# Kernel tuning notes

Measured on AMD Instinct MI355X. Metric: run time of the kernel, lower is better.

The kernel has to match this reference:

```python
import jax, jax.numpy as jnp
import numpy as np

D_MODEL = 768
N_HEADS = 12
HEAD_DIM = D_MODEL // N_HEADS


def setup_inputs() -> dict:
    key = jax.random.key(0)
    ks = jax.random.split(key, 9)
    B, S = 2, 2048
    x = jax.random.normal(ks[0], (B, S, D_MODEL), dtype=jnp.float32)
    s = 1.0 / np.sqrt(D_MODEL)
    Wq = jax.random.normal(ks[1], (D_MODEL, D_MODEL), dtype=jnp.float32) * s
    bq = jax.random.normal(ks[2], (D_MODEL,), dtype=jnp.float32) * 0.01
    Wk = jax.random.normal(ks[3], (D_MODEL, D_MODEL), dtype=jnp.float32) * s
    bk = jax.random.normal(ks[4], (D_MODEL,), dtype=jnp.float32) * 0.01
    Wv = jax.random.normal(ks[5], (D_MODEL, D_MODEL), dtype=jnp.float32) * s
    bv = jax.random.normal(ks[6], (D_MODEL,), dtype=jnp.float32) * 0.01
    Wo = jax.random.normal(ks[7], (D_MODEL, D_MODEL), dtype=jnp.float32) * s
    bo = jax.random.normal(ks[8], (D_MODEL,), dtype=jnp.float32) * 0.01
    return {"x": x, "Wq": Wq, "bq": bq, "Wk": Wk, "bk": bk,
            "Wv": Wv, "bv": bv, "Wo": Wo, "bo": bo}


def reference(x, Wq, bq, Wk, bk, Wv, bv, Wo, bo):
    B, S, _ = x.shape
    H, Dh = N_HEADS, HEAD_DIM
    # Projections (torch Linear: x @ W.T + b; here W stored as [in, out])
    q = (x @ Wq + bq).reshape(B, S, H, Dh)
    k = (x @ Wk + bk).reshape(B, S, H, Dh)
    v = (x @ Wv + bv).reshape(B, S, H, Dh)
    scale = 1.0 / jnp.sqrt(jnp.float32(Dh))
    # NOTE: source applies no causal mask despite the class name.
    scores = jnp.einsum('bqhd,bkhd->bhqk', q, k) * scale
    attn = jax.nn.softmax(scores, axis=-1)
    out = jnp.einsum('bhqk,bkhd->bqhd', attn, v).reshape(B, S, H * Dh)
    return out @ Wo + bo
```

## Files before the change

kernel.cpp:

```cpp
#include <hip/hip_runtime.h>

typedef unsigned short u16;
typedef __fp16 halfx2 __attribute__((ext_vector_type(2)));
typedef __fp16 halfx8 __attribute__((ext_vector_type(8)));
typedef float floatx4 __attribute__((ext_vector_type(4)));
typedef unsigned short u16x4 __attribute__((ext_vector_type(4)));
typedef unsigned short u16x8 __attribute__((ext_vector_type(8)));

#define D_MODEL 768
#define NH 12
#define DH 64
#define SEQ 2048
#define BATCH 2
#define MTOK 4096
#define DQKV 2304

__device__ __forceinline__ u16 f2h(float f) {
    __fp16 h = (__fp16)f;
    return __builtin_bit_cast(u16, h);
}

__device__ __forceinline__ void gload_lds16(const void* g, void* l) {
    __builtin_amdgcn_global_load_lds(
        (const __attribute__((address_space(1))) void*)g,
        (__attribute__((address_space(3))) void*)l, 16, 0, 0);
}


__global__ __launch_bounds__(256) void wprep_kernel(const float* __restrict__ Wq, const float* __restrict__ Wk,
                                                    const float* __restrict__ Wv, const float* __restrict__ Wo,
                                                    u16* __restrict__ WqkvT, u16* __restrict__ WoT) {
    __shared__ u16 t[64][72];
    int bid = blockIdx.x;
    int tid = threadIdx.x;
    int z = bid / 144;
    int t2 = bid % 144;
    int k0 = (t2 / 12) * 64, n0 = (t2 % 12) * 64;
    const float* W = (z == 0) ? Wq : (z == 1) ? Wk : (z == 2) ? Wv : Wo;
    u16* dst = (z < 3) ? (WqkvT + (size_t)z * 768 * 768) : WoT;
#pragma unroll
    for (int p = 0; p < 16; ++p) {
        int idx = p * 256 + tid;
        int kr = idx >> 6, nc = idx & 63;
        t[kr][nc] = f2h(W[(size_t)(k0 + kr) * 768 + n0 + nc]);
    }
    __syncthreads();
#pragma unroll
    for (int p = 0; p < 16; ++p) {
        int idx = p * 256 + tid;
        int nr = idx >> 6, kc = idx & 63;
        dst[(size_t)(n0 + nr) * 768 + k0 + kc] = t[kc][nr];
    }
}


__global__ __launch_bounds__(256) void gemm_qkv(const float* __restrict__ x, const u16* __restrict__ Bt,
                                                const float* __restrict__ bq, const float* __restrict__ bk,
                                                const float* __restrict__ bv,
                                                u16* __restrict__ qP, u16* __restrict__ kP,
                                                u16* __restrict__ vTout) {
    const int tid = threadIdx.x;
    const int wid = tid >> 6;
    const int lane = tid & 63;
    const int qd = lane >> 4;
    const int l15 = lane & 15;

    const int tn = blockIdx.x * 128;
    const int tm = blockIdx.y * 64;
    const int wm = (wid >> 1) * 32;
    const int wn = (wid & 1) * 64;

    __shared__ alignas(16) u16 As[64 * 64];
    __shared__ alignas(16) u16 Bs[128 * 64];

    floatx4 acc[2][4];
#pragma unroll
    for (int i = 0; i < 2; ++i)
#pragma unroll
        for (int j = 0; j < 4; ++j) acc[i][j] = (floatx4)(0.0f);

    int ar[2], abl[2];
#pragma unroll
    for (int rd = 0; rd < 2; ++rd) {
        int s = rd * 256 + tid;
        ar[rd] = s >> 3;
        abl[rd] = (s & 7) ^ (ar[rd] & 7);
    }
    const u16* Bg[4];
#pragma unroll
    for (int rd = 0; rd < 4; ++rd) {
        int s = rd * 256 + tid;
        int r = s >> 3, bl = (s & 7) ^ (r & 7);
        Bg[rd] = Bt + (size_t)(tn + r) * 768 + bl * 8;
    }

    for (int kb = 0; kb < 768; kb += 64) {
        __syncthreads();
#pragma unroll
        for (int rd = 0; rd < 2; ++rd) {
            const float* src = x + (size_t)(tm + ar[rd]) * 768 + kb + abl[rd] * 8;
            float4 v0 = *(const float4*)src;
            float4 v1 = *(const float4*)(src + 4);
            union { u16x8 u; halfx2 h[4]; } pk;
            pk.h[0] = __builtin_amdgcn_cvt_pkrtz(v0.x, v0.y);
            pk.h[1] = __builtin_amdgcn_cvt_pkrtz(v0.z, v0.w);
            pk.h[2] = __builtin_amdgcn_cvt_pkrtz(v1.x, v1.y);
            pk.h[3] = __builtin_amdgcn_cvt_pkrtz(v1.z, v1.w);
            *(u16x8*)(As + (size_t)(rd * 256 + tid) * 8) = pk.u;
        }
#pragma unroll
        for (int rd = 0; rd < 4; ++rd)
            gload_lds16(Bg[rd] + kb, Bs + (size_t)(rd * 256 + tid) * 8);
        __syncthreads();

#pragma unroll
        for (int ks = 0; ks < 2; ++ks) {
            halfx8 af[2], bf[4];
#pragma unroll
            for (int i = 0; i < 2; ++i) {
                int r = wm + i * 16 + l15;
                af[i] = *(const halfx8*)(As + r * 64 + (((ks * 4 + qd) ^ (r & 7)) * 8));
            }
#pragma unroll
            for (int j = 0; j < 4; ++j) {
                int r2 = wn + j * 16 + l15;
                bf[j] = *(const halfx8*)(Bs + r2 * 64 + (((ks * 4 + qd) ^ (r2 & 7)) * 8));
            }
#pragma unroll
            for (int i = 0; i < 2; ++i)
#pragma unroll
                for (int j = 0; j < 4; ++j)
                    acc[i][j] = __builtin_amdgcn_mfma_f32_16x16x32_f16(af[i], bf[j], acc[i][j], 0, 0, 0);
        }
    }

    const float cscale = 0.125f * 1.44269504088896340736f;
    const int rgn = (tn < 768) ? 0 : (tn < 1536) ? 1 : 2;
    const float* bsrc = (rgn == 0) ? bq : (rgn == 1) ? bk : bv;
#pragma unroll
    for (int j = 0; j < 4; ++j) {
        int col = tn + wn + j * 16 + l15;
        int cl = col - rgn * 768;
        float bvv = bsrc[cl];
        int h = cl >> 6, d = cl & 63;
#pragma unroll
        for (int i = 0; i < 2; ++i) {
            int row0 = tm + wm + i * 16 + qd * 4;
            int b = row0 >> 11, s0 = row0 & 2047;
            u16x4 pk;
#pragma unroll
            for (int r = 0; r < 4; ++r) {
                float v = acc[i][j][r] + bvv;
                if (rgn == 0) v *= cscale;
                pk[r] = f2h(v);
            }
            if (rgn == 2) {
                *(u16x4*)(vTout + ((size_t)(b * NH + h) * 64 + d) * SEQ + s0) = pk;
            } else {
                u16* dst = (rgn == 0) ? qP : kP;
#pragma unroll
                for (int r = 0; r < 4; ++r)
                    dst[((size_t)(b * NH + h) * SEQ + s0 + r) * DH + d] = pk[r];
            }
        }
    }
}


__global__ __launch_bounds__(256, 2) void attn_kernel(const u16* __restrict__ qP, const u16* __restrict__ kP,
                                                      const u16* __restrict__ vT, u16* __restrict__ attn) {
    const int tid = threadIdx.x;
    const int wid = tid >> 6;
    const int lane = tid & 63;
    const int qd = lane >> 4;
    const int l15 = lane & 15;

    const int bh = blockIdx.x;
    const int b = bh / NH, h = bh % NH;
    const int q0 = blockIdx.y * 64;

    __shared__ alignas(16) u16 smem[9216];
    u16* ps = smem + wid * 2304;

    halfx8 aq[4][2];
#pragma unroll
    for (int jn = 0; jn < 4; ++jn)
#pragma unroll
        for (int ks = 0; ks < 2; ++ks)
            aq[jn][ks] = *(const halfx8*)(qP + (size_t)(bh * SEQ + q0 + jn * 16 + l15) * DH + ks * 32 + qd * 8);

    halfx8 ones;
#pragma unroll
    for (int j = 0; j < 8; ++j) ones[j] = (__fp16)1.0f;

    floatx4 o[4][4];
#pragma unroll
    for (int ip = 0; ip < 4; ++ip)
#pragma unroll
        for (int jn = 0; jn < 4; ++jn) o[ip][jn] = (floatx4)(0.0f);
    floatx4 lsum[4];
#pragma unroll
    for (int jn = 0; jn < 4; ++jn) lsum[jn] = (floatx4)(0.0f);

    const u16* kbase = kP + (size_t)(bh * SEQ + wid * 32 + l15) * DH + qd * 8;
    const u16* vbase = vT + (size_t)(bh * 64 + l15) * SEQ + wid * 32 + qd * 8;

    halfx8 akn[2][2], avc[4];
#pragma unroll
    for (int mi = 0; mi < 2; ++mi)
#pragma unroll
        for (int ks = 0; ks < 2; ++ks)
            akn[mi][ks] = *(const halfx8*)(kbase + (size_t)(mi * 16) * DH + ks * 32);
#pragma unroll
    for (int ip = 0; ip < 4; ++ip)
        avc[ip] = *(const halfx8*)(vbase + (size_t)(ip * 16) * SEQ);

    floatx4 sc[2][4];
#pragma unroll
    for (int mi = 0; mi < 2; ++mi)
#pragma unroll
        for (int jn = 0; jn < 4; ++jn) sc[mi][jn] = (floatx4)(0.0f);
#pragma unroll
    for (int ks = 0; ks < 2; ++ks)
#pragma unroll
        for (int mi = 0; mi < 2; ++mi)
#pragma unroll
            for (int jn = 0; jn < 4; ++jn)
                sc[mi][jn] = __builtin_amdgcn_mfma_f32_16x16x32_f16(akn[mi][ks], aq[jn][ks], sc[mi][jn], 0, 0, 0);

    for (int kt = 0; kt < 16; ++kt) {
        int ktn = (kt + 1) & 15;
        halfx8 avn[4];
#pragma unroll
        for (int mi = 0; mi < 2; ++mi)
#pragma unroll
            for (int ks = 0; ks < 2; ++ks)
                akn[mi][ks] = *(const halfx8*)(kbase + (size_t)(ktn * 128 + mi * 16) * DH + ks * 32);
#pragma unroll
        for (int ip = 0; ip < 4; ++ip)
            avn[ip] = *(const halfx8*)(vbase + (size_t)(ip * 16) * SEQ + ktn * 128);

#pragma unroll
        for (int mi = 0; mi < 2; ++mi)
#pragma unroll
            for (int jn = 0; jn < 4; ++jn) {
                float p0 = __builtin_amdgcn_exp2f(sc[mi][jn][0]);
                float p1 = __builtin_amdgcn_exp2f(sc[mi][jn][1]);
                float p2 = __builtin_amdgcn_exp2f(sc[mi][jn][2]);
                float p3 = __builtin_amdgcn_exp2f(sc[mi][jn][3]);
                union { u16x4 u; halfx2 h[2]; } pk;
                pk.h[0] = __builtin_amdgcn_cvt_pkrtz(p0, p1);
                pk.h[1] = __builtin_amdgcn_cvt_pkrtz(p2, p3);
                *(u16x4*)(ps + (jn * 16 + l15) * 36 + mi * 16 + qd * 4) = pk.u;
            }

        floatx4 scn[2][4];
#pragma unroll
        for (int mi = 0; mi < 2; ++mi)
#pragma unroll
            for (int jn = 0; jn < 4; ++jn) scn[mi][jn] = (floatx4)(0.0f);
#pragma unroll
        for (int ks = 0; ks < 2; ++ks)
#pragma unroll
            for (int mi = 0; mi < 2; ++mi)
#pragma unroll
                for (int jn = 0; jn < 4; ++jn)
                    scn[mi][jn] = __builtin_amdgcn_mfma_f32_16x16x32_f16(akn[mi][ks], aq[jn][ks], scn[mi][jn], 0, 0, 0);

        halfx8 bp[4];
#pragma unroll
        for (int jn = 0; jn < 4; ++jn) {
            union { halfx8 h8; u16x4 u4[2]; } bpu;
            bpu.u4[0] = *(const u16x4*)(ps + (jn * 16 + l15) * 36 + qd * 8);
            bpu.u4[1] = *(const u16x4*)(ps + (jn * 16 + l15) * 36 + qd * 8 + 4);
            bp[jn] = bpu.h8;
        }

#pragma unroll
        for (int jn = 0; jn < 4; ++jn)
            lsum[jn] = __builtin_amdgcn_mfma_f32_16x16x32_f16(ones, bp[jn], lsum[jn], 0, 0, 0);
#pragma unroll
        for (int ip = 0; ip < 4; ++ip)
#pragma unroll
            for (int jn = 0; jn < 4; ++jn)
                o[ip][jn] = __builtin_amdgcn_mfma_f32_16x16x32_f16(avc[ip], bp[jn], o[ip][jn], 0, 0, 0);

#pragma unroll
        for (int ip = 0; ip < 4; ++ip) avc[ip] = avn[ip];
#pragma unroll
        for (int mi = 0; mi < 2; ++mi)
#pragma unroll
            for (int jn = 0; jn < 4; ++jn) sc[mi][jn] = scn[mi][jn];
    }

    float* Oacc = (float*)smem;
    float* la = (float*)smem + 4352;

    __syncthreads();
    if (wid == 0) {
#pragma unroll
        for (int jn = 0; jn < 4; ++jn) {
            int q = jn * 16 + l15;
#pragma unroll
            for (int ip = 0; ip < 4; ++ip)
                *(floatx4*)(Oacc + q * 68 + ip * 16 + qd * 4) = o[ip][jn];
            if (qd == 0) la[q] = lsum[jn][0];
        }
    }
    for (int w = 1; w < 4; ++w) {
        __syncthreads();
        if (wid == w) {
#pragma unroll
            for (int jn = 0; jn < 4; ++jn) {
                int q = jn * 16 + l15;
#pragma unroll
                for (int ip = 0; ip < 4; ++ip) {
                    float* p = Oacc + q * 68 + ip * 16 + qd * 4;
                    *(floatx4*)p = *(floatx4*)p + o[ip][jn];
                }
                if (qd == 0) la[q] += lsum[jn][0];
            }
        }
    }
    __syncthreads();

    {
        int q = tid >> 2, d0 = (tid & 3) * 16;
        float inv = __builtin_amdgcn_rcpf(la[q]);
        const float* op = Oacc + q * 68 + d0;
        u16x8 pk0, pk1;
#pragma unroll
        for (int r = 0; r < 8; ++r) pk0[r] = f2h(op[r] * inv);
#pragma unroll
        for (int r = 0; r < 8; ++r) pk1[r] = f2h(op[8 + r] * inv);
        u16* dst = attn + (size_t)(b * SEQ + q0 + q) * D_MODEL + h * DH + d0;
        *(u16x8*)dst = pk0;
        *(u16x8*)(dst + 8) = pk1;
    }
}


__global__ __launch_bounds__(256) void gemm_out(const u16* __restrict__ A, const u16* __restrict__ Bt,
                                                const float* __restrict__ bias, float* __restrict__ Cout) {
    const int tid = threadIdx.x;
    const int wid = tid >> 6;
    const int lane = tid & 63;
    const int qd = lane >> 4;
    const int l15 = lane & 15;

    const int tn = blockIdx.x * 64;
    const int tm = blockIdx.y * 64;
    const int wm = (wid >> 1) * 32;
    const int wn = (wid & 1) * 32;

    __shared__ alignas(16) u16 As[64 * 64];
    __shared__ alignas(16) u16 Bs[64 * 64];

    floatx4 acc[2][2];
#pragma unroll
    for (int i = 0; i < 2; ++i)
#pragma unroll
        for (int j = 0; j < 2; ++j) acc[i][j] = (floatx4)(0.0f);

    const u16* Ag[2];
    const u16* Bg[2];
#pragma unroll
    for (int rd = 0; rd < 2; ++rd) {
        int s = rd * 256 + tid;
        int r = s >> 3, bl = (s & 7) ^ (r & 7);
        Ag[rd] = A + (size_t)(tm + r) * 768 + bl * 8;
        Bg[rd] = Bt + (size_t)(tn + r) * 768 + bl * 8;
    }

    for (int kb = 0; kb < 768; kb += 64) {
        __syncthreads();
#pragma unroll
        for (int rd = 0; rd < 2; ++rd) {
            gload_lds16(Ag[rd] + kb, As + (size_t)(rd * 256 + tid) * 8);
            gload_lds16(Bg[rd] + kb, Bs + (size_t)(rd * 256 + tid) * 8);
        }
        __syncthreads();

#pragma unroll
        for (int ks = 0; ks < 2; ++ks) {
            halfx8 af[2], bf[2];
#pragma unroll
            for (int i = 0; i < 2; ++i) {
                int r = wm + i * 16 + l15;
                af[i] = *(const halfx8*)(As + r * 64 + (((ks * 4 + qd) ^ (r & 7)) * 8));
                int r2 = wn + i * 16 + l15;
                bf[i] = *(const halfx8*)(Bs + r2 * 64 + (((ks * 4 + qd) ^ (r2 & 7)) * 8));
            }
#pragma unroll
            for (int i = 0; i < 2; ++i)
#pragma unroll
                for (int j = 0; j < 2; ++j)
                    acc[i][j] = __builtin_amdgcn_mfma_f32_16x16x32_f16(af[i], bf[j], acc[i][j], 0, 0, 0);
        }
    }

#pragma unroll
    for (int j = 0; j < 2; ++j) {
        int col = tn + wn + j * 16 + l15;
        float bv = bias[col];
#pragma unroll
        for (int i = 0; i < 2; ++i) {
            int row0 = tm + wm + i * 16 + qd * 4;
#pragma unroll
            for (int r = 0; r < 4; ++r)
                Cout[(size_t)(row0 + r) * 768 + col] = acc[i][j][r] + bv;
        }
    }
}


extern "C" void kernel_launch(void* const* d_in, const int* in_sizes, int n_in,
                              void* d_out, int out_size, void* d_ws, size_t ws_size,
                              hipStream_t stream) {
    const float* x  = (const float*)d_in[0];
    const float* Wq = (const float*)d_in[1];
    const float* bq = (const float*)d_in[2];
    const float* Wk = (const float*)d_in[3];
    const float* bk = (const float*)d_in[4];
    const float* Wv = (const float*)d_in[5];
    const float* bv = (const float*)d_in[6];
    const float* Wo = (const float*)d_in[7];
    const float* bo = (const float*)d_in[8];

    char* ws = (char*)d_ws;
    size_t off = 0;
    auto take = [&](size_t bytes) -> char* {
        char* p = ws + off;
        off += (bytes + 255) & ~(size_t)255;
        return p;
    };
    u16* WqkvT = (u16*)take((size_t)DQKV * D_MODEL * 2);
    u16* WoT   = (u16*)take((size_t)D_MODEL * D_MODEL * 2);
    u16* qP    = (u16*)take((size_t)MTOK * D_MODEL * 2);
    u16* kP    = (u16*)take((size_t)MTOK * D_MODEL * 2);
    u16* vTb   = (u16*)take((size_t)BATCH * NH * DH * SEQ * 2);
    u16* attn  = (u16*)take((size_t)MTOK * D_MODEL * 2);

    wprep_kernel<<<576, 256, 0, stream>>>(Wq, Wk, Wv, Wo, WqkvT, WoT);
    gemm_qkv<<<dim3(DQKV / 128, MTOK / 64), 256, 0, stream>>>(x, WqkvT, bq, bk, bv, qP, kP, vTb);
    attn_kernel<<<dim3(BATCH * NH, SEQ / 64), 256, 0, stream>>>(qP, kP, vTb, attn);
    gemm_out<<<dim3(D_MODEL / 64, MTOK / 64), 256, 0, stream>>>(attn, WoT, bo, (float*)d_out);
}
```

Baseline: 180.1 us.

## Pre-convert x to fp16 and halve attention query tile for occupancy

The weight-prep kernel now also converts x to fp16 into a scratch buffer (aliasing the attn buffer), so the QKV GEMM can load A tiles with direct global-to-LDS loads instead of loading fp32, converting and storing per k-step. The attention kernel processes 32 queries per block instead of 64, which halves registers and LDS per block, raises the launch-bounds occupancy hint to 3, and doubles the grid. Its key loop is unrolled by two with ping-pong score and V buffers to drop register copies. The trade-off is more K/V reloads per query and an extra fp16 pass over x.

```diff
diff --git a/kernel.cpp b/kernel.cpp
--- a/kernel.cpp
+++ b/kernel.cpp
@@ -29,10 +29,24 @@
 
 __global__ __launch_bounds__(256) void wprep_kernel(const float* __restrict__ Wq, const float* __restrict__ Wk,
                                                     const float* __restrict__ Wv, const float* __restrict__ Wo,
-                                                    u16* __restrict__ WqkvT, u16* __restrict__ WoT) {
+                                                    const float* __restrict__ x,
+                                                    u16* __restrict__ WqkvT, u16* __restrict__ WoT,
+                                                    u16* __restrict__ xh) {
     __shared__ u16 t[64][72];
     int bid = blockIdx.x;
     int tid = threadIdx.x;
+    if (bid >= 576) {
+        int idx = (bid - 576) * 2048 + tid * 8;
+        float4 v0 = *(const float4*)(x + idx);
+        float4 v1 = *(const float4*)(x + idx + 4);
+        union { u16x8 u; halfx2 h[4]; } pk;
+        pk.h[0] = __builtin_amdgcn_cvt_pkrtz(v0.x, v0.y);
+        pk.h[1] = __builtin_amdgcn_cvt_pkrtz(v0.z, v0.w);
+        pk.h[2] = __builtin_amdgcn_cvt_pkrtz(v1.x, v1.y);
+        pk.h[3] = __builtin_amdgcn_cvt_pkrtz(v1.z, v1.w);
+        *(u16x8*)(xh + idx) = pk.u;
+        return;
+    }
     int z = bid / 144;
     int t2 = bid % 144;
     int k0 = (t2 / 12) * 64, n0 = (t2 % 12) * 64;
@@ -54,7 +68,7 @@
 }
 
 
-__global__ __launch_bounds__(256) void gemm_qkv(const float* __restrict__ x, const u16* __restrict__ Bt,
+__global__ __launch_bounds__(256) void gemm_qkv(const u16* __restrict__ xh, const u16* __restrict__ Bt,
                                                 const float* __restrict__ bq, const float* __restrict__ bk,
                                                 const float* __restrict__ bv,
                                                 u16* __restrict__ qP, u16* __restrict__ kP,
@@ -79,12 +93,12 @@
 #pragma unroll
         for (int j = 0; j < 4; ++j) acc[i][j] = (floatx4)(0.0f);
 
-    int ar[2], abl[2];
+    const u16* Ag[2];
 #pragma unroll
     for (int rd = 0; rd < 2; ++rd) {
         int s = rd * 256 + tid;
-        ar[rd] = s >> 3;
-        abl[rd] = (s & 7) ^ (ar[rd] & 7);
+        int r = s >> 3, bl = (s & 7) ^ (r & 7);
+        Ag[rd] = xh + (size_t)(tm + r) * 768 + bl * 8;
     }
     const u16* Bg[4];
 #pragma unroll
@@ -97,17 +111,8 @@
     for (int kb = 0; kb < 768; kb += 64) {
         __syncthreads();
 #pragma unroll
-        for (int rd = 0; rd < 2; ++rd) {
-            const float* src = x + (size_t)(tm + ar[rd]) * 768 + kb + abl[rd] * 8;
-            float4 v0 = *(const float4*)src;
-            float4 v1 = *(const float4*)(src + 4);
-            union { u16x8 u; halfx2 h[4]; } pk;
-            pk.h[0] = __builtin_amdgcn_cvt_pkrtz(v0.x, v0.y);
-            pk.h[1] = __builtin_amdgcn_cvt_pkrtz(v0.z, v0.w);
-            pk.h[2] = __builtin_amdgcn_cvt_pkrtz(v1.x, v1.y);
-            pk.h[3] = __builtin_amdgcn_cvt_pkrtz(v1.z, v1.w);
-            *(u16x8*)(As + (size_t)(rd * 256 + tid) * 8) = pk.u;
-        }
+        for (int rd = 0; rd < 2; ++rd)
+            gload_lds16(Ag[rd] + kb, As + (size_t)(rd * 256 + tid) * 8);
 #pragma unroll
         for (int rd = 0; rd < 4; ++rd)
             gload_lds16(Bg[rd] + kb, Bs + (size_t)(rd * 256 + tid) * 8);
@@ -167,7 +172,7 @@
 }
 
 
-__global__ __launch_bounds__(256, 2) void attn_kernel(const u16* __restrict__ qP, const u16* __restrict__ kP,
+__global__ __launch_bounds__(256, 3) void attn_kernel(const u16* __restrict__ qP, const u16* __restrict__ kP,
                                                       const u16* __restrict__ vT, u16* __restrict__ attn) {
     const int tid = threadIdx.x;
     const int wid = tid >> 6;
@@ -177,14 +182,14 @@
 
     const int bh = blockIdx.x;
     const int b = bh / NH, h = bh % NH;
-    const int q0 = blockIdx.y * 64;
-
-    __shared__ alignas(16) u16 smem[9216];
-    u16* ps = smem + wid * 2304;
-
-    halfx8 aq[4][2];
-#pragma unroll
-    for (int jn = 0; jn < 4; ++jn)
+    const int q0 = blockIdx.y * 32;
+
+    __shared__ alignas(16) u16 smem[4608];
+    u16* ps = smem + wid * 1152;
+
+    halfx8 aq[2][2];
+#pragma unroll
+    for (int jn = 0; jn < 2; ++jn)
 #pragma unroll
         for (int ks = 0; ks < 2; ++ks)
             aq[jn][ks] = *(const halfx8*)(qP + (size_t)(bh * SEQ + q0 + jn * 16 + l15) * DH + ks * 32 + qd * 8);
@@ -193,83 +198,88 @@
 #pragma unroll
     for (int j = 0; j < 8; ++j) ones[j] = (__fp16)1.0f;
 
-    floatx4 o[4][4];
+    floatx4 o[4][2];
 #pragma unroll
     for (int ip = 0; ip < 4; ++ip)
 #pragma unroll
-        for (int jn = 0; jn < 4; ++jn) o[ip][jn] = (floatx4)(0.0f);
-    floatx4 lsum[4];
-#pragma unroll
-    for (int jn = 0; jn < 4; ++jn) lsum[jn] = (floatx4)(0.0f);
+        for (int jn = 0; jn < 2; ++jn) o[ip][jn] = (floatx4)(0.0f);
+    floatx4 lsum[2];
+#pragma unroll
+    for (int jn = 0; jn < 2; ++jn) lsum[jn] = (floatx4)(0.0f);
 
     const u16* kbase = kP + (size_t)(bh * SEQ + wid * 32 + l15) * DH + qd * 8;
     const u16* vbase = vT + (size_t)(bh * 64 + l15) * SEQ + wid * 32 + qd * 8;
 
-    halfx8 akn[2][2], avc[4];
-#pragma unroll
-    for (int mi = 0; mi < 2; ++mi)
+    halfx8 avA[4], avB[4];
+    floatx4 scA[2][2], scB[2][2];
+    {
+        halfx8 akp[2][2];
+#pragma unroll
+        for (int mi = 0; mi < 2; ++mi)
+#pragma unroll
+            for (int ks = 0; ks < 2; ++ks)
+                akp[mi][ks] = *(const halfx8*)(kbase + (size_t)(mi * 16) * DH + ks * 32);
+#pragma unroll
+        for (int ip = 0; ip < 4; ++ip)
+            avA[ip] = *(const halfx8*)(vbase + (size_t)(ip * 16) * SEQ);
+
+#pragma unroll
+        for (int mi = 0; mi < 2; ++mi)
+#pragma unroll
+            for (int jn = 0; jn < 2; ++jn) scA[mi][jn] = (floatx4)(0.0f);
 #pragma unroll
         for (int ks = 0; ks < 2; ++ks)
-            akn[mi][ks] = *(const halfx8*)(kbase + (size_t)(mi * 16) * DH + ks * 32);
-#pragma unroll
-    for (int ip = 0; ip < 4; ++ip)
-        avc[ip] = *(const halfx8*)(vbase + (size_t)(ip * 16) * SEQ);
-
-    floatx4 sc[2][4];
-#pragma unroll
-    for (int mi = 0; mi < 2; ++mi)
-#pragma unroll
-        for (int jn = 0; jn < 4; ++jn) sc[mi][jn] = (floatx4)(0.0f);
-#pragma unroll
-    for (int ks = 0; ks < 2; ++ks)
+#pragma unroll
+            for (int mi = 0; mi < 2; ++mi)
+#pragma unroll
+                for (int jn = 0; jn < 2; ++jn)
+                    scA[mi][jn] = __builtin_amdgcn_mfma_f32_16x16x32_f16(akp[mi][ks], aq[jn][ks], scA[mi][jn], 0, 0, 0);
+    }
+
+    auto body = [&](int kt,
+                    floatx4 (&scC)[2][2], floatx4 (&scN)[2][2],
+                    halfx8 (&avU)[4], halfx8 (&avF)[4]) {
+        const int kt1 = (kt + 1) & 15;
+
+        halfx8 akn[2][2];
 #pragma unroll
         for (int mi = 0; mi < 2; ++mi)
 #pragma unroll
-            for (int jn = 0; jn < 4; ++jn)
-                sc[mi][jn] = __builtin_amdgcn_mfma_f32_16x16x32_f16(akn[mi][ks], aq[jn][ks], sc[mi][jn], 0, 0, 0);
-
-    for (int kt = 0; kt < 16; ++kt) {
-        int ktn = (kt + 1) & 15;
-        halfx8 avn[4];
+            for (int ks = 0; ks < 2; ++ks)
+                akn[mi][ks] = *(const halfx8*)(kbase + (size_t)(kt1 * 128 + mi * 16) * DH + ks * 32);
+#pragma unroll
+        for (int ip = 0; ip < 4; ++ip)
+            avF[ip] = *(const halfx8*)(vbase + (size_t)(ip * 16) * SEQ + kt1 * 128);
+
 #pragma unroll
         for (int mi = 0; mi < 2; ++mi)
 #pragma unroll
-            for (int ks = 0; ks < 2; ++ks)
-                akn[mi][ks] = *(const halfx8*)(kbase + (size_t)(ktn * 128 + mi * 16) * DH + ks * 32);
-#pragma unroll
-        for (int ip = 0; ip < 4; ++ip)
-            avn[ip] = *(const halfx8*)(vbase + (size_t)(ip * 16) * SEQ + ktn * 128);
-
-#pragma unroll
-        for (int mi = 0; mi < 2; ++mi)
-#pragma unroll
-            for (int jn = 0; jn < 4; ++jn) {
-                float p0 = __builtin_amdgcn_exp2f(sc[mi][jn][0]);
-                float p1 = __builtin_amdgcn_exp2f(sc[mi][jn][1]);
-                float p2 = __builtin_amdgcn_exp2f(sc[mi][jn][2]);
-                float p3 = __builtin_amdgcn_exp2f(sc[mi][jn][3]);
+            for (int jn = 0; jn < 2; ++jn) {
+                float p0 = __builtin_amdgcn_exp2f(scC[mi][jn][0]);
+                float p1 = __builtin_amdgcn_exp2f(scC[mi][jn][1]);
+                float p2 = __builtin_amdgcn_exp2f(scC[mi][jn][2]);
+                float p3 = __builtin_amdgcn_exp2f(scC[mi][jn][3]);
                 union { u16x4 u; halfx2 h[2]; } pk;
                 pk.h[0] = __builtin_amdgcn_cvt_pkrtz(p0, p1);
                 pk.h[1] = __builtin_amdgcn_cvt_pkrtz(p2, p3);
                 *(u16x4*)(ps + (jn * 16 + l15) * 36 + mi * 16 + qd * 4) = pk.u;
             }
 
-        floatx4 scn[2][4];
 #pragma unroll
         for (int mi = 0; mi < 2; ++mi)
 #pragma unroll
-            for (int jn = 0; jn < 4; ++jn) scn[mi][jn] = (floatx4)(0.0f);
+            for (int jn = 0; jn < 2; ++jn) scN[mi][jn] = (floatx4)(0.0f);
 #pragma unroll
         for (int ks = 0; ks < 2; ++ks)
 #pragma unroll
             for (int mi = 0; mi < 2; ++mi)
 #pragma unroll
-                for (int jn = 0; jn < 4; ++jn)
-                    scn[mi][jn] = __builtin_amdgcn_mfma_f32_16x16x32_f16(akn[mi][ks], aq[jn][ks], scn[mi][jn], 0, 0, 0);
-
-        halfx8 bp[4];
-#pragma unroll
-        for (int jn = 0; jn < 4; ++jn) {
+                for (int jn = 0; jn < 2; ++jn)
+                    scN[mi][jn] = __builtin_amdgcn_mfma_f32_16x16x32_f16(akn[mi][ks], aq[jn][ks], scN[mi][jn], 0, 0, 0);
+
+        halfx8 bp[2];
+#pragma unroll
+        for (int jn = 0; jn < 2; ++jn) {
             union { halfx8 h8; u16x4 u4[2]; } bpu;
             bpu.u4[0] = *(const u16x4*)(ps + (jn * 16 + l15) * 36 + qd * 8);
             bpu.u4[1] = *(const u16x4*)(ps + (jn * 16 + l15) * 36 + qd * 8 + 4);
@@ -277,29 +287,27 @@
         }
 
 #pragma unroll
-        for (int jn = 0; jn < 4; ++jn)
+        for (int jn = 0; jn < 2; ++jn)
             lsum[jn] = __builtin_amdgcn_mfma_f32_16x16x32_f16(ones, bp[jn], lsum[jn], 0, 0, 0);
 #pragma unroll
         for (int ip = 0; ip < 4; ++ip)
 #pragma unroll
-            for (int jn = 0; jn < 4; ++jn)
-                o[ip][jn] = __builtin_amdgcn_mfma_f32_16x16x32_f16(avc[ip], bp[jn], o[ip][jn], 0, 0, 0);
-
-#pragma unroll
-        for (int ip = 0; ip < 4; ++ip) avc[ip] = avn[ip];
-#pragma unroll
-        for (int mi = 0; mi < 2; ++mi)
-#pragma unroll
-            for (int jn = 0; jn < 4; ++jn) sc[mi][jn] = scn[mi][jn];
+            for (int jn = 0; jn < 2; ++jn)
+                o[ip][jn] = __builtin_amdgcn_mfma_f32_16x16x32_f16(avU[ip], bp[jn], o[ip][jn], 0, 0, 0);
+    };
+
+    for (int kt = 0; kt < 16; kt += 2) {
+        body(kt,     scA, scB, avA, avB);
+        body(kt + 1, scB, scA, avB, avA);
     }
 
     float* Oacc = (float*)smem;
-    float* la = (float*)smem + 4352;
+    float* la = (float*)smem + 2176;
 
     __syncthreads();
     if (wid == 0) {
 #pragma unroll
-        for (int jn = 0; jn < 4; ++jn) {
+        for (int jn = 0; jn < 2; ++jn) {
             int q = jn * 16 + l15;
 #pragma unroll
             for (int ip = 0; ip < 4; ++ip)
@@ -311,7 +319,7 @@
         __syncthreads();
         if (wid == w) {
 #pragma unroll
-            for (int jn = 0; jn < 4; ++jn) {
+            for (int jn = 0; jn < 2; ++jn) {
                 int q = jn * 16 + l15;
 #pragma unroll
                 for (int ip = 0; ip < 4; ++ip) {
@@ -325,17 +333,14 @@
     __syncthreads();
 
     {
-        int q = tid >> 2, d0 = (tid & 3) * 16;
+        int q = tid >> 3, d0 = (tid & 7) * 8;
         float inv = __builtin_amdgcn_rcpf(la[q]);
         const float* op = Oacc + q * 68 + d0;
-        u16x8 pk0, pk1;
-#pragma unroll
-        for (int r = 0; r < 8; ++r) pk0[r] = f2h(op[r] * inv);
-#pragma unroll
-        for (int r = 0; r < 8; ++r) pk1[r] = f2h(op[8 + r] * inv);
+        u16x8 pk;
+#pragma unroll
+        for (int r = 0; r < 8; ++r) pk[r] = f2h(op[r] * inv);
         u16* dst = attn + (size_t)(b * SEQ + q0 + q) * D_MODEL + h * DH + d0;
-        *(u16x8*)dst = pk0;
-        *(u16x8*)(dst + 8) = pk1;
+        *(u16x8*)dst = pk;
     }
 }
 
@@ -440,9 +445,10 @@
     u16* kP    = (u16*)take((size_t)MTOK * D_MODEL * 2);
     u16* vTb   = (u16*)take((size_t)BATCH * NH * DH * SEQ * 2);
     u16* attn  = (u16*)take((size_t)MTOK * D_MODEL * 2);
-
-    wprep_kernel<<<576, 256, 0, stream>>>(Wq, Wk, Wv, Wo, WqkvT, WoT);
-    gemm_qkv<<<dim3(DQKV / 128, MTOK / 64), 256, 0, stream>>>(x, WqkvT, bq, bk, bv, qP, kP, vTb);
-    attn_kernel<<<dim3(BATCH * NH, SEQ / 64), 256, 0, stream>>>(qP, kP, vTb, attn);
+    u16* xh = attn;
+
+    wprep_kernel<<<576 + (MTOK * D_MODEL / 2048), 256, 0, stream>>>(Wq, Wk, Wv, Wo, x, WqkvT, WoT, xh);
+    gemm_qkv<<<dim3(DQKV / 128, MTOK / 64), 256, 0, stream>>>(xh, WqkvT, bq, bk, bv, qP, kP, vTb);
+    attn_kernel<<<dim3(BATCH * NH, SEQ / 32), 256, 0, stream>>>(qP, kP, vTb, attn);
     gemm_out<<<dim3(D_MODEL / 64, MTOK / 64), 256, 0, stream>>>(attn, WoT, bo, (float*)d_out);
 }
```

After: 217.2 us. +20.6%, slower.
